# Optimization experiments

Hardware: AMD Instinct MI355X
Metric: run time of the kernel (lower is better)

Reference implementation:

```python
import jax, jax.numpy as jnp
from jax import lax
import numpy as np

DIM = 768      # model dim
NL = 12        # num mamba layers
DS = 16        # d_state
DI = 1536      # d_inner = 2*dim
DC = 4         # d_conv
P = 16         # patch size
IMG = 256
NP = (IMG // P) ** 2  # 256 patches
GS = 5         # KAN grid_size
SO = 3         # KAN spline_order
NK = NL // 3   # 4 KAN layers
BATCH = 32


def setup_inputs() -> dict:
    key = jax.random.key(0)
    ks = jax.random.split(key, 16)
    def n(k, shape, s=0.02):
        return jax.random.normal(k, shape, jnp.float32) * s
    return {
        "x": jax.random.normal(ks[0], (BATCH, 3, IMG, IMG), jnp.float32),
        "patch_w": n(ks[1], (DIM, 3, P, P)),
        "patch_b": jnp.zeros((DIM,), jnp.float32),
        "pos_embed": n(ks[2], (1, NP, DIM)),
        "in_proj_w": n(ks[3], (NL, 2 * DI, DIM)),
        "conv_w": n(ks[4], (NL, DI, 1, DC), 0.1),
        "conv_b": jnp.zeros((NL, DI), jnp.float32),
        "x_proj_w": n(ks[5], (NL, 2 * DS, DI)),
        "dt_proj_w": n(ks[6], (NL, DS, DI)),
        "dt_proj_b": jnp.zeros((NL, DS), jnp.float32),
        "A_log": jnp.tile(jnp.log(jnp.arange(1, DS + 1, dtype=jnp.float32)), (NL, 1)),
        "D_param": jnp.ones((NL, DI), jnp.float32),
        "out_proj_w": n(ks[7], (NL, DIM, DI)),
        "kan_base_w": n(ks[8], (NK, DIM, DIM)),
        "kan_coeff": n(ks[9], (NK, DIM, DIM, GS + SO), 0.1),
        "kan_bias": n(ks[10], (NK, DIM), 0.01),
        "norm_w": jnp.ones((DIM,), jnp.float32),
        "norm_b": jnp.zeros((DIM,), jnp.float32),
    }


def _mamba_block(x, in_w, cw, cb, xpw, dtw, dtb, alog, Dp, ow):
    Bsz, L, _ = x.shape
    xr = jnp.einsum('bld,ed->ble', x, in_w)              # [B,L,2*DI]
    x1, res = xr[..., :DI], xr[..., DI:]
    # causal depthwise conv (pad d_conv-1 on left, truncate to L)
    xc = lax.conv_general_dilated(
        x1.transpose(0, 2, 1), cw, (1,), [(DC - 1, 0)],
        feature_group_count=DI,
        dimension_numbers=('NCH', 'OIH', 'NCH')) + cb[None, :, None]
    x1 = jax.nn.silu(xc.transpose(0, 2, 1))              # [B,L,DI]
    x_dbl = jnp.einsum('bld,ed->ble', x1, xpw)           # [B,L,2*DS]
    Bp = x_dbl[..., DS:]                                 # dt half of x_proj is discarded (as in torch)
    dt = jax.nn.softplus(jnp.einsum('bld,nd->bln', x1, dtw) + dtb)  # [B,L,DS]
    A = -jnp.exp(alog)                                   # [DS]
    Ad = jnp.exp(A * dt)                                 # [B,L,DS]
    u = x1[..., :DI // DS].mean(-1)                      # [B,L]
    Bd = dt * Bp * u[..., None]                          # [B,L,DS]
    def step(s, ab):
        a, b = ab
        s = s * a + b
        return s, s
    _, ys = lax.scan(step, jnp.zeros((Bsz, DS), x.dtype),
                     (Ad.transpose(1, 0, 2), Bd.transpose(1, 0, 2)))
    y = ys.transpose(1, 0, 2)                            # [B,L,DS]
    y = jnp.repeat(y, DI // DS, axis=-1)                 # n -> (n d)
    y = y + x1 * Dp
    y = y * jax.nn.silu(res)
    return jnp.einsum('bld,ed->ble', y, ow)              # [B,L,DIM]


def _kan(xf, bw, coeff, bias):
    base = xf @ bw.T + bias
    grid = jnp.linspace(-1.0, 1.0, GS + 1)
    denom = grid[1:] - grid[:-1] + 1e-8
    xs = (xf[..., None] - grid[:-1]) / denom             # [M,DIM,GS]
    basis = jnp.where((xs >= 0) & (xs < 1), xs, 0.0)
    return base + jnp.einsum('bik,oik->bo', basis, coeff[:, :, :GS])


def reference(x, patch_w, patch_b, pos_embed, in_proj_w, conv_w, conv_b,
              x_proj_w, dt_proj_w, dt_proj_b, A_log, D_param, out_proj_w,
              kan_base_w, kan_coeff, kan_bias, norm_w, norm_b):
    Bsz = x.shape[0]
    h = lax.conv_general_dilated(
        x, patch_w, (P, P), 'VALID',
        dimension_numbers=('NCHW', 'OIHW', 'NCHW')) + patch_b[None, :, None, None]
    h = h.transpose(0, 2, 3, 1).reshape(Bsz, NP, DIM) + pos_embed
    for i in range(NL):
        h = _mamba_block(h, in_proj_w[i], conv_w[i], conv_b[i], x_proj_w[i],
                         dt_proj_w[i], dt_proj_b[i], A_log[i], D_param[i], out_proj_w[i])
        if i % 3 == 2 and i // 3 < NK:
            j = i // 3
            hf = h.reshape(-1, DIM)
            h = _kan(hf, kan_base_w[j], kan_coeff[j], kan_bias[j]).reshape(Bsz, NP, DIM) + h
    mu = h.mean(-1, keepdims=True)
    var = ((h - mu) ** 2).mean(-1, keepdims=True)
    return (h - mu) / jnp.sqrt(var + 1e-5) * norm_w + norm_b
```

## Files before the change

### kernel.cpp

```cpp
#include <hip/hip_runtime.h>

#define BATCH 32
#define NPATCH 256
#define MROWS (BATCH * NPATCH)
#define DIM 768
#define DI 1536
#define DS 16

typedef __bf16 bf16_t;
typedef __attribute__((ext_vector_type(8))) __bf16 bf16x8;
typedef __attribute__((ext_vector_type(4))) float floatx4;

__device__ __forceinline__ float bf2f(unsigned short u) {
    union { unsigned int i; float f; } v; v.i = ((unsigned int)u) << 16; return v.f;
}
__device__ __forceinline__ unsigned short f2bf(float f) {
    union { float f; unsigned int i; } u; u.f = f;
    unsigned int r = u.i + 0x7FFFu + ((u.i >> 16) & 1u);
    return (unsigned short)(r >> 16);
}
__device__ __forceinline__ float ldin(const void* p, int i, int bf) {
    if (bf) return bf2f(((const unsigned short*)p)[i]);
    return ((const float*)p)[i];
}
__device__ __forceinline__ float4 ldin4(const void* p, int i, int bf) {
    if (bf) {
        ushort4 u = *(const ushort4*)((const unsigned short*)p + i);
        return make_float4(bf2f(u.x), bf2f(u.y), bf2f(u.z), bf2f(u.w));
    }
    return *(const float4*)((const float*)p + i);
}
__device__ __forceinline__ float siluf(float x) { return x / (1.0f + expf(-x)); }

__global__ void detect_k(const void* alog, int* flag) {
    if (threadIdx.x == 0 && blockIdx.x == 0) {
        float v = ((const float*)alog)[1];
        flag[0] = (fabsf(v - 0.69314718f) < 0.01f) ? 0 : 1;
    }
}

__global__ __launch_bounds__(256) void cvt4_k(const int* __restrict__ flag,
                                              const void* __restrict__ in,
                                              unsigned short* __restrict__ out, int n4) {
    int i = blockIdx.x * 256 + threadIdx.x;
    if (i >= n4) return;
    float4 v = ldin4(in, i * 4, flag[0]);
    ushort4 o;
    o.x = f2bf(v.x); o.y = f2bf(v.y); o.z = f2bf(v.z); o.w = f2bf(v.w);
    *(ushort4*)(out + i * 4) = o;
}

__global__ __launch_bounds__(256) void kcoef_k(const int* __restrict__ flag,
                                               const void* __restrict__ co,
                                               bf16_t* __restrict__ out) {
    int idx = blockIdx.x * 256 + threadIdx.x;
    int bf = flag[0];
    int j = idx / (768 * 3840);
    int r = idx - j * (768 * 3840);
    int n = r / 3840;
    int kk = r - n * 3840;
    int i = kk / 5, k5 = kk - i * 5;
    out[idx] = (bf16_t)ldin(co, ((j * 768 + n) * 768 + i) * 8 + k5, bf);
}

__global__ __launch_bounds__(256) void wproj_k(const int* __restrict__ flag,
                                               const void* __restrict__ dtw,
                                               const void* __restrict__ xpw,
                                               bf16_t* __restrict__ w2) {
    int idx = blockIdx.x * 256 + threadIdx.x;
    int bf = flag[0];
    int i = idx / (128 * 1536);
    int r = idx - i * (128 * 1536);
    int n = r / 1536, k = r - n * 1536;
    float v;
    if (n < 16)       v = ldin(dtw, (i * 16 + n) * 1536 + k, bf);
    else if (n < 32)  v = ldin(xpw, (i * 32 + n) * 1536 + k, bf);
    else if (n == 32) v = (k < 96) ? (1.0f / 96.0f) : 0.0f;
    else              v = 0.0f;
    w2[idx] = (bf16_t)v;
}

__global__ __launch_bounds__(256) void cvtconv_k(const int* __restrict__ flag,
                                                 const void* __restrict__ cw,
                                                 bf16_t* __restrict__ cwr) {
    int idx = blockIdx.x * 256 + threadIdx.x;
    int bf = flag[0];
    int i = idx / (4 * 1536);
    int r = idx - i * (4 * 1536);
    int k = r / 1536, c = r - k * 1536;
    cwr[idx] = (bf16_t)ldin(cw, i * 1536 * 4 + c * 4 + k, bf);
}

__global__ __launch_bounds__(256) void basis_k(const bf16_t* __restrict__ h,
                                               bf16_t* __restrict__ bas) {
    int idx = blockIdx.x * 256 + threadIdx.x;
    int m = idx / 96, i8 = (idx - m * 96) * 8;
    bf16x8 hv = *(const bf16x8*)(h + (size_t)m * 768 + i8);
    union { bf16_t a[40]; bf16x8 v[5]; } ob;
#pragma unroll
    for (int ii = 0; ii < 8; ii++) {
        float xv = (float)hv[ii];
#pragma unroll
        for (int k5 = 0; k5 < 5; k5++) {
            float tt = (xv + 1.0f - 0.4f * (float)k5) * 2.5f;
            ob.a[ii * 5 + k5] = (bf16_t)((tt >= 0.0f && tt < 1.0f) ? tt : 0.0f);
        }
    }
    bf16_t* op = bas + (size_t)m * 3840 + (size_t)i8 * 5;
#pragma unroll
    for (int j = 0; j < 5; j++) *(bf16x8*)(op + j * 8) = ob.v[j];
}

__global__ __launch_bounds__(256) void im2col_k(const int* __restrict__ flag,
                                                const void* __restrict__ x,
                                                bf16_t* __restrict__ xp) {
    int idx = blockIdx.x * 256 + threadIdx.x;
    int bf = flag[0];
    int m = idx / 768, kc = idx - m * 768;
    int b = m >> 8, p = m & 255;
    int py = p >> 4, px = p & 15;
    int c = kc >> 8, rr = kc & 255;
    int ky = rr >> 4, kx = rr & 15;
    int src = ((b * 3 + c) * 256 + py * 16 + ky) * 256 + px * 16 + kx;
    xp[idx] = (bf16_t)ldin(x, src, bf);
}

__global__ __launch_bounds__(256) void mgemm_k(
    const bf16_t* __restrict__ A, int lda,
    const bf16_t* __restrict__ W, int ldw,
    bf16_t* __restrict__ C, int ldc,
    int K, int mode, int gx,
    const int* __restrict__ flag,
    const void* __restrict__ bias, int boff,
    const void* __restrict__ aux, int aoff,
    const bf16_t* __restrict__ H, int ldh,
    float* __restrict__ dtu) {
    __shared__ bf16_t sm[2][2 * 128 * 64];
    const int t = threadIdx.x;
    const int lane = t & 63, wave = t >> 6;
    const int wm = wave >> 1, wn = wave & 1;

    int m0, n0, kbeg, kend;
    if (mode == 5) {
        int mt = blockIdx.x >> 2, ks = blockIdx.x & 3;
        m0 = mt << 7; n0 = 0;
        int KS = K >> 2;
        kbeg = ks * KS; kend = kbeg + KS;
    } else {
        const int bid = blockIdx.x;
        const int xcd = bid & 7, l = bid >> 3;
        const int w = gx < 8 ? gx : 8;
        const int cb8 = w * 8;
        const int ch = l / cb8, rem = l - ch * cb8;
        const int mi = rem / w, ni = rem - mi * w;
        m0 = (xcd * 8 + mi) << 7;
        n0 = (ch * w + ni) << 7;
        kbeg = 0; kend = K;
    }

    const int srow = t >> 3;
    const int colperm = (((t & 7) ^ (srow & 7)) << 3);
    const bf16_t* gA[4]; const bf16_t* gB[4];
#pragma unroll
    for (int r = 0; r < 4; r++) {
        gA[r] = A + (size_t)(m0 + r * 32 + srow) * lda + colperm;
        gB[r] = W + (size_t)(n0 + r * 32 + srow) * ldw + colperm;
    }

    floatx4 acc[4][4];
#pragma unroll
    for (int i = 0; i < 4; i++)
#pragma unroll
        for (int j = 0; j < 4; j++) acc[i][j] = (floatx4){0.f, 0.f, 0.f, 0.f};

    const int kq = lane >> 4;
    const int mr = lane & 15;

    auto stage = [&](int buf, int kt) {
        char* sa = (char*)&sm[buf][0];
#pragma unroll
        for (int r = 0; r < 4; r++) {
            const int off = r * 4096 + wave * 1024;
            __builtin_amdgcn_global_load_lds(
                (const __attribute__((address_space(1))) unsigned int*)(gA[r] + kt),
                (__attribute__((address_space(3))) unsigned int*)(sa + off), 16, 0, 0);
            __builtin_amdgcn_global_load_lds(
                (const __attribute__((address_space(1))) unsigned int*)(gB[r] + kt),
                (__attribute__((address_space(3))) unsigned int*)(sa + 16384 + off), 16, 0, 0);
        }
    };

    auto compute = [&](int buf) {
        const bf16_t* sAc = &sm[buf][0];
        const bf16_t* sBc = sAc + 128 * 64;
#pragma unroll
        for (int half = 0; half < 2; half++) {
            const int cb = half * 4 + kq;
            if (mode == 5) {
                if (wn == 0) {
                    bf16x8 af[4], bw3[3];
#pragma unroll
                    for (int i = 0; i < 4; i++) {
                        int rw = wm * 64 + i * 16 + mr;
                        af[i] = *(const bf16x8*)(sAc + rw * 64 + ((cb ^ (rw & 7)) << 3));
                    }
#pragma unroll
                    for (int j = 0; j < 3; j++) {
                        int rw = j * 16 + mr;
                        bw3[j] = *(const bf16x8*)(sBc + rw * 64 + ((cb ^ (rw & 7)) << 3));
                    }
#pragma unroll
                    for (int i = 0; i < 4; i++)
#pragma unroll
                        for (int j = 0; j < 3; j++)
                            acc[i][j] = __builtin_amdgcn_mfma_f32_16x16x32_bf16(af[i], bw3[j], acc[i][j], 0, 0, 0);
                }
            } else {
                bf16x8 af[4], bw[4];
#pragma unroll
                for (int i = 0; i < 4; i++) {
                    int rw = wm * 64 + i * 16 + mr;
                    af[i] = *(const bf16x8*)(sAc + rw * 64 + ((cb ^ (rw & 7)) << 3));
                }
#pragma unroll
                for (int j = 0; j < 4; j++) {
                    int rw = wn * 64 + j * 16 + mr;
                    bw[j] = *(const bf16x8*)(sBc + rw * 64 + ((cb ^ (rw & 7)) << 3));
                }
#pragma unroll
                for (int i = 0; i < 4; i++)
#pragma unroll
                    for (int j = 0; j < 4; j++)
                        acc[i][j] = __builtin_amdgcn_mfma_f32_16x16x32_bf16(af[i], bw[j], acc[i][j], 0, 0, 0);
            }
        }
    };

    stage(0, kbeg);
    int cur = 0;
    for (int kt = kbeg; kt < kend; kt += 64) {
        if (kt + 64 < kend) {
            stage(cur ^ 1, kt + 64);
            asm volatile("s_waitcnt vmcnt(8)" ::: "memory");
        } else {
            asm volatile("s_waitcnt vmcnt(0)" ::: "memory");
        }
        asm volatile("s_barrier" ::: "memory");
        compute(cur);
        asm volatile("s_barrier" ::: "memory");
        cur ^= 1;
    }

    const int col = lane & 15;
    const int rq = (lane >> 4) * 4;

    if (mode == 5) {
        if (wn == 0) {
            int ks = blockIdx.x & 3;
            float* dst = dtu + (size_t)ks * (MROWS * 64);
#pragma unroll
            for (int i = 0; i < 4; i++) {
#pragma unroll
                for (int reg = 0; reg < 4; reg++) {
                    int gm = m0 + wm * 64 + i * 16 + rq + reg;
#pragma unroll
                    for (int j = 0; j < 3; j++) {
                        int gn = j * 16 + col;
                        if (gn <= 32)
                            dst[(size_t)gm * 64 + gn] = acc[i][j][reg];
                    }
                }
            }
        }
        return;
    }

    const int bff = (mode == 1 || mode == 2) ? flag[0] : 0;
#pragma unroll
    for (int i = 0; i < 4; i++) {
#pragma unroll
        for (int reg = 0; reg < 4; reg++) {
            int gm = m0 + wm * 64 + i * 16 + rq + reg;
#pragma unroll
            for (int j = 0; j < 4; j++) {
                int gn = n0 + wn * 64 + j * 16 + col;
                float v = acc[i][j][reg];
                if (mode == 1) v += ldin(bias, boff + gn, bff) + ldin(aux, aoff + (gm & 255) * 768 + gn, bff);
                else if (mode == 2) v += ldin(bias, boff + gn, bff);
                else if (mode == 3) v += (float)C[(size_t)gm * ldc + gn] + (float)H[(size_t)gm * ldh + gn];
                C[(size_t)gm * ldc + gn] = (bf16_t)v;
            }
        }
    }
}

__global__ __launch_bounds__(512, 2) void mgemm256_k(
    const bf16_t* __restrict__ A, int lda,
    const bf16_t* __restrict__ W, int ldw,
    bf16_t* __restrict__ C, int ldc,
    int K) {
    __shared__ bf16_t sm[2][2 * 256 * 64];
    const int t = threadIdx.x;
    const int lane = t & 63, wave = t >> 6;
    const int wm = wave >> 2, wn = wave & 3;

    const int bid = blockIdx.x;
    const int xcd = bid & 7, l = bid >> 3;
    const int mi = l & 3, ni = l >> 2;
    const int m0 = (xcd * 4 + mi) << 8;
    const int n0 = ni << 8;

    const int srow = t >> 3;
    const int colperm = (((t & 7) ^ (srow & 7)) << 3);
    const bf16_t* gA[4]; const bf16_t* gB[4];
#pragma unroll
    for (int r = 0; r < 4; r++) {
        gA[r] = A + (size_t)(m0 + r * 64 + srow) * lda + colperm;
        gB[r] = W + (size_t)(n0 + r * 64 + srow) * ldw + colperm;
    }

    floatx4 acc[8][4];
#pragma unroll
    for (int i = 0; i < 8; i++)
#pragma unroll
        for (int j = 0; j < 4; j++) acc[i][j] = (floatx4){0.f, 0.f, 0.f, 0.f};

    const int kq = lane >> 4;
    const int mr = lane & 15;

    auto stage = [&](int buf, int kt) {
        char* sa = (char*)&sm[buf][0];
#pragma unroll
        for (int r = 0; r < 4; r++) {
            const int off = (r * 512 + t) * 16;
            __builtin_amdgcn_global_load_lds(
                (const __attribute__((address_space(1))) unsigned int*)(gA[r] + kt),
                (__attribute__((address_space(3))) unsigned int*)(sa + off), 16, 0, 0);
            __builtin_amdgcn_global_load_lds(
                (const __attribute__((address_space(1))) unsigned int*)(gB[r] + kt),
                (__attribute__((address_space(3))) unsigned int*)(sa + 32768 + off), 16, 0, 0);
        }
    };

    stage(0, 0);
    int cur = 0;
    for (int kt = 0; kt < K; kt += 64) {
        asm volatile("s_waitcnt vmcnt(0)" ::: "memory");
        asm volatile("s_barrier" ::: "memory");
        if (kt + 64 < K) stage(cur ^ 1, kt + 64);
        const bf16_t* sAc = &sm[cur][0];
        const bf16_t* sBc = sAc + 256 * 64;
#pragma unroll
        for (int half = 0; half < 2; half++) {
            const int cb = half * 4 + kq;
            bf16x8 bw[4];
#pragma unroll
            for (int j = 0; j < 4; j++) {
                int rw = wn * 64 + j * 16 + mr;
                bw[j] = *(const bf16x8*)(sBc + rw * 64 + ((cb ^ (rw & 7)) << 3));
            }
#pragma unroll
            for (int ib = 0; ib < 2; ib++) {
                bf16x8 af[4];
#pragma unroll
                for (int i2 = 0; i2 < 4; i2++) {
                    int rw = wm * 128 + (ib * 4 + i2) * 16 + mr;
                    af[i2] = *(const bf16x8*)(sAc + rw * 64 + ((cb ^ (rw & 7)) << 3));
                }
                __builtin_amdgcn_s_setprio(1);
#pragma unroll
                for (int i2 = 0; i2 < 4; i2++)
#pragma unroll
                    for (int j = 0; j < 4; j++)
                        acc[ib * 4 + i2][j] = __builtin_amdgcn_mfma_f32_16x16x32_bf16(
                            af[i2], bw[j], acc[ib * 4 + i2][j], 0, 0, 0);
                __builtin_amdgcn_s_setprio(0);
                asm volatile("s_barrier" ::: "memory");
            }
        }
        cur ^= 1;
    }

    const int col = lane & 15;
    const int rq = (lane >> 4) * 4;
#pragma unroll
    for (int i = 0; i < 8; i++) {
#pragma unroll
        for (int reg = 0; reg < 4; reg++) {
            int gm = m0 + wm * 128 + i * 16 + rq + reg;
#pragma unroll
            for (int j = 0; j < 4; j++) {
                int gn = n0 + wn * 64 + j * 16 + col;
                C[(size_t)gm * ldc + gn] = (bf16_t)acc[i][j][reg];
            }
        }
    }
}

__global__ __launch_bounds__(256) void conv_k(const int* __restrict__ flag,
                                              const bf16_t* __restrict__ xr,
                                              const bf16_t* __restrict__ cwr,
                                              const void* __restrict__ cb, int cbo,
                                              bf16_t* __restrict__ xc) {
    int idx = blockIdx.x * 256 + threadIdx.x;
    int bf = flag[0];
    int m = idx / 192, c8 = (idx - m * 192) * 8;
    int l = m & 255;
    float acc[8];
    float4 b0 = ldin4(cb, cbo + c8, bf), b1 = ldin4(cb, cbo + c8 + 4, bf);
    acc[0] = b0.x; acc[1] = b0.y; acc[2] = b0.z; acc[3] = b0.w;
    acc[4] = b1.x; acc[5] = b1.y; acc[6] = b1.z; acc[7] = b1.w;
#pragma unroll
    for (int k = 0; k < 4; k++) {
        if (l + k - 3 >= 0) {
            bf16x8 xv = *(const bf16x8*)(xr + (size_t)(m + k - 3) * 3072 + c8);
            bf16x8 wv = *(const bf16x8*)(cwr + k * 1536 + c8);
#pragma unroll
            for (int j = 0; j < 8; j++) acc[j] += (float)xv[j] * (float)wv[j];
        }
    }
    bf16x8 o;
#pragma unroll
    for (int j = 0; j < 8; j++) o[j] = (bf16_t)siluf(acc[j]);
    *(bf16x8*)(xc + (size_t)m * 1536 + c8) = o;
}

__global__ __launch_bounds__(256) void scan_k(const int* __restrict__ flag,
                                              const float* __restrict__ dtu,
                                              const void* __restrict__ dtb, int dtbo,
                                              const void* __restrict__ alog, int alo,
                                              float* __restrict__ ys) {
    int wid = (blockIdx.x * 256 + threadIdx.x) >> 6;
    int lane = threadIdx.x & 63;
    int b = wid >> 4, s = wid & 15;
    int bf = flag[0];
    float dtbv = ldin(dtb, dtbo + s, bf);
    float Av = -expf(ldin(alog, alo + s, bf));
    const float* pb = dtu + (size_t)b * (256 * 64);
    float* yo = ys + (size_t)b * (256 * 16);
    float Aj[4], Bj[4];
    float A = 1.0f, Bv = 0.0f;
#pragma unroll
    for (int j = 0; j < 4; j++) {
        int l = lane * 4 + j;
        float rdt = dtbv, rBp = 0.0f, ru = 0.0f;
#pragma unroll
        for (int ks = 0; ks < 4; ks++) {
            const float* q = pb + (size_t)ks * (MROWS * 64) + (size_t)l * 64;
            rdt += q[s];
            rBp += q[16 + s];
            ru  += q[32];
        }
        float dt = (rdt > 20.0f) ? rdt : log1pf(expf(rdt));
        float a = expf(Av * dt);
        float bb = dt * rBp * ru;
        Bv = Bv * a + bb;
        A = A * a;
        Aj[j] = A; Bj[j] = Bv;
    }
#pragma unroll
    for (int off = 1; off < 64; off <<= 1) {
        float pa = __shfl_up(A, off);
        float pb2 = __shfl_up(Bv, off);
        if (lane >= off) { Bv = pb2 * A + Bv; A = pa * A; }
    }
    float ex = __shfl_up(Bv, 1);
    if (lane == 0) ex = 0.0f;
#pragma unroll
    for (int j = 0; j < 4; j++) {
        int l = lane * 4 + j;
        yo[l * 16 + s] = Aj[j] * ex + Bj[j];
    }
}

__global__ __launch_bounds__(256) void gate_k(const int* __restrict__ flag,
                                              const float* __restrict__ ys,
                                              bf16_t* __restrict__ xc,
                                              const bf16_t* __restrict__ xr,
                                              const void* __restrict__ Dp, int dpo) {
    int idx = blockIdx.x * 256 + threadIdx.x;
    int bf = flag[0];
    int m = idx / 192, d8 = (idx - m * 192) * 8;
    float yv = ys[m * 16 + d8 / 96];
    bf16x8 rv = *(const bf16x8*)(xr + (size_t)m * 3072 + 1536 + d8);
    bf16x8 xv = *(const bf16x8*)(xc + (size_t)m * 1536 + d8);
    float4 dp0 = ldin4(Dp, dpo + d8, bf), dp1 = ldin4(Dp, dpo + d8 + 4, bf);
    float dpv[8] = {dp0.x, dp0.y, dp0.z, dp0.w, dp1.x, dp1.y, dp1.z, dp1.w};
    bf16x8 o;
#pragma unroll
    for (int j = 0; j < 8; j++) {
        float v = yv + (float)xv[j] * dpv[j];
        o[j] = (bf16_t)(v * siluf((float)rv[j]));
    }
    *(bf16x8*)(xc + (size_t)m * 1536 + d8) = o;
}

__global__ __launch_bounds__(256) void lnorm_k(const int* __restrict__ flag,
                                               const bf16_t* __restrict__ h,
                                               const void* __restrict__ nw,
                                               const void* __restrict__ nb,
                                               void* __restrict__ out) {
    __shared__ float ls[4];
    int bf = flag[0];
    int m = blockIdx.x, t = threadIdx.x;
    const bf16_t* row = h + (size_t)m * 768;
    float v0 = (float)row[t], v1 = (float)row[t + 256], v2 = (float)row[t + 512];
    float s = v0 + v1 + v2;
#pragma unroll
    for (int o = 32; o; o >>= 1) s += __shfl_xor(s, o);
    if ((t & 63) == 0) ls[t >> 6] = s;
    __syncthreads();
    float mu = (ls[0] + ls[1] + ls[2] + ls[3]) * (1.0f / 768.0f);
    __syncthreads();
    float d0 = v0 - mu, d1 = v1 - mu, d2 = v2 - mu;
    float q = d0 * d0 + d1 * d1 + d2 * d2;
#pragma unroll
    for (int o = 32; o; o >>= 1) q += __shfl_xor(q, o);
    if ((t & 63) == 0) ls[t >> 6] = q;
    __syncthreads();
    float var = (ls[0] + ls[1] + ls[2] + ls[3]) * (1.0f / 768.0f);
    float inv = rsqrtf(var + 1e-5f);
    float vv[3] = {d0, d1, d2};
#pragma unroll
    for (int j = 0; j < 3; j++) {
        int colx = t + 256 * j;
        float o = vv[j] * inv * ldin(nw, colx, bf) + ldin(nb, colx, bf);
        size_t oi = (size_t)m * 768 + colx;
        if (bf) ((unsigned short*)out)[oi] = f2bf(o);
        else    ((float*)out)[oi] = o;
    }
}

extern "C" void kernel_launch(void* const* d_in, const int* in_sizes, int n_in,
                              void* d_out, int out_size, void* d_ws, size_t ws_size,
                              hipStream_t stream) {
    const void* x        = d_in[0];
    const void* patch_w  = d_in[1];
    const void* patch_b  = d_in[2];
    const void* pos      = d_in[3];
    const void* in_w     = d_in[4];
    const void* conv_w   = d_in[5];
    const void* conv_b   = d_in[6];
    const void* xpw      = d_in[7];
    const void* dtw      = d_in[8];
    const void* dtb      = d_in[9];
    const void* alog     = d_in[10];
    const void* Dp       = d_in[11];
    const void* out_w    = d_in[12];
    const void* kbw      = d_in[13];
    const void* kcoef    = d_in[14];
    const void* kbias    = d_in[15];
    const void* nw       = d_in[16];
    const void* nb       = d_in[17];

    char* base = (char*)d_ws;
    size_t off = 0;
    int* flag = (int*)base;                          off += 256;
    float* dtu  = (float*)(base + off);              off += (size_t)4 * MROWS * 64 * 4;
    float* ysb  = (float*)(base + off);              off += (size_t)MROWS * 16 * 4;
    bf16_t* hA  = (bf16_t*)(base + off);             off += (size_t)MROWS * DIM * 2;
    bf16_t* hB  = (bf16_t*)(base + off);             off += (size_t)MROWS * DIM * 2;
    bf16_t* xr  = (bf16_t*)(base + off);             off += (size_t)MROWS * 2 * DI * 2;
    bf16_t* xc  = (bf16_t*)(base + off);             off += (size_t)MROWS * DI * 2;
    bf16_t* wpatch = (bf16_t*)(base + off);          off += (size_t)DIM * DIM * 2;
    bf16_t* win  = (bf16_t*)(base + off);            off += (size_t)12 * 2 * DI * DIM * 2;
    bf16_t* wout = (bf16_t*)(base + off);            off += (size_t)12 * DIM * DI * 2;
    bf16_t* wkbw = (bf16_t*)(base + off);            off += (size_t)4 * DIM * DIM * 2;
    bf16_t* wkco = (bf16_t*)(base + off);            off += (size_t)4 * DIM * 3840 * 2;
    bf16_t* w2   = (bf16_t*)(base + off);            off += (size_t)12 * 128 * DI * 2;
    bf16_t* cwr  = (bf16_t*)(base + off);            off += (size_t)12 * 4 * DI * 2;
    bf16_t* basis = xr;
    bf16_t* im2c  = xr;

    detect_k<<<1, 64, 0, stream>>>(alog, flag);

    cvt4_k<<<(DIM * DIM / 4 + 255) / 256, 256, 0, stream>>>(flag, patch_w, (unsigned short*)wpatch, DIM * DIM / 4);
    cvt4_k<<<(12 * 2 * DI * DIM / 4 + 255) / 256, 256, 0, stream>>>(flag, in_w, (unsigned short*)win, 12 * 2 * DI * DIM / 4);
    cvt4_k<<<(12 * DIM * DI / 4 + 255) / 256, 256, 0, stream>>>(flag, out_w, (unsigned short*)wout, 12 * DIM * DI / 4);
    cvt4_k<<<(4 * DIM * DIM / 4 + 255) / 256, 256, 0, stream>>>(flag, kbw, (unsigned short*)wkbw, 4 * DIM * DIM / 4);
    kcoef_k<<<4 * DIM * 3840 / 256, 256, 0, stream>>>(flag, kcoef, wkco);
    wproj_k<<<12 * 128 * DI / 256, 256, 0, stream>>>(flag, dtw, xpw, w2);
    cvtconv_k<<<12 * 4 * DI / 256, 256, 0, stream>>>(flag, conv_w, cwr);

    im2col_k<<<(MROWS * DIM) / 256, 256, 0, stream>>>(flag, x, im2c);
    mgemm_k<<<6 * 64, 256, 0, stream>>>(
        im2c, DIM, wpatch, DIM, hA, DIM, DIM, 1, 6,
        flag, patch_b, 0, pos, 0, nullptr, 0, nullptr);

    bf16_t* hcur = hA;
    bf16_t* hoth = hB;
    for (int i = 0; i < 12; i++) {
        mgemm256_k<<<384, 512, 0, stream>>>(
            hcur, DIM, win + (size_t)i * 2 * DI * DIM, DIM, xr, 2 * DI, DIM);
        conv_k<<<(MROWS * 192) / 256, 256, 0, stream>>>(
            flag, xr, cwr + (size_t)i * 4 * DI, conv_b, i * DI, xc);
        mgemm_k<<<256, 256, 0, stream>>>(
            xc, DI, w2 + (size_t)i * 128 * DI, DI, nullptr, 128, DI, 5, 1,
            flag, nullptr, 0, nullptr, 0, nullptr, 0, dtu);
        scan_k<<<128, 256, 0, stream>>>(flag, dtu, dtb, i * DS, alog, i * DS, ysb);
        gate_k<<<(MROWS * 192) / 256, 256, 0, stream>>>(
            flag, ysb, xc, xr, Dp, i * DI);
        mgemm_k<<<6 * 64, 256, 0, stream>>>(
            xc, DI, wout + (size_t)i * DIM * DI, DI, hcur, DIM, DI, 0, 6,
            flag, nullptr, 0, nullptr, 0, nullptr, 0, nullptr);
        if (i % 3 == 2) {
            int j = i / 3;
            mgemm_k<<<6 * 64, 256, 0, stream>>>(
                hcur, DIM, wkbw + (size_t)j * DIM * DIM, DIM, hoth, DIM, DIM, 2, 6,
                flag, kbias, j * DIM, nullptr, 0, nullptr, 0, nullptr);
            basis_k<<<(MROWS * 96) / 256, 256, 0, stream>>>(hcur, basis);
            mgemm_k<<<6 * 64, 256, 0, stream>>>(
                basis, 3840, wkco + (size_t)j * DIM * 3840, 3840, hoth, DIM, 3840, 3, 6,
                flag, nullptr, 0, nullptr, 0, hcur, DIM, nullptr);
            bf16_t* tmp = hcur; hcur = hoth; hoth = tmp;
        }
    }

    lnorm_k<<<MROWS, 256, 0, stream>>>(flag, hcur, nw, nb, d_out);
}
```

Before: 2.592 ms.

## Restructure in_proj GEMM pipeline and compute two rows per conv thread

The 256-tile GEMM now issues the next stage's global-to-LDS loads before waiting, using a partial vmcnt wait so prefetch overlaps compute. It drops the per-half barriers and the setprio hints, and relaxes launch bounds to one block per CU, giving the compiler more registers. The depthwise conv kernel now has each thread produce two consecutive rows, reusing the weights and overlapping input rows to cut redundant loads, and launches half as many threads. The risks are lower occupancy in the GEMM and a wait count that may not match the actual number of outstanding loads, which could read LDS before it is filled.

Result: faster. 2.515 ms (-3.0%).

```diff
diff --git a/kernel.cpp b/kernel.cpp
--- a/kernel.cpp
+++ b/kernel.cpp
@@ -294,7 +294,7 @@
     }
 }
 
-__global__ __launch_bounds__(512, 2) void mgemm256_k(
+__global__ __launch_bounds__(512, 1) void mgemm256_k(
     const bf16_t* __restrict__ A, int lda,
     const bf16_t* __restrict__ W, int ldw,
     bf16_t* __restrict__ C, int ldc,
@@ -342,13 +342,8 @@
         }
     };
 
-    stage(0, 0);
-    int cur = 0;
-    for (int kt = 0; kt < K; kt += 64) {
-        asm volatile("s_waitcnt vmcnt(0)" ::: "memory");
-        asm volatile("s_barrier" ::: "memory");
-        if (kt + 64 < K) stage(cur ^ 1, kt + 64);
-        const bf16_t* sAc = &sm[cur][0];
+    auto compute = [&](int buf) {
+        const bf16_t* sAc = &sm[buf][0];
         const bf16_t* sBc = sAc + 256 * 64;
 #pragma unroll
         for (int half = 0; half < 2; half++) {
@@ -367,17 +362,28 @@
                     int rw = wm * 128 + (ib * 4 + i2) * 16 + mr;
                     af[i2] = *(const bf16x8*)(sAc + rw * 64 + ((cb ^ (rw & 7)) << 3));
                 }
-                __builtin_amdgcn_s_setprio(1);
 #pragma unroll
                 for (int i2 = 0; i2 < 4; i2++)
 #pragma unroll
                     for (int j = 0; j < 4; j++)
                         acc[ib * 4 + i2][j] = __builtin_amdgcn_mfma_f32_16x16x32_bf16(
                             af[i2], bw[j], acc[ib * 4 + i2][j], 0, 0, 0);
-                __builtin_amdgcn_s_setprio(0);
-                asm volatile("s_barrier" ::: "memory");
             }
         }
+    };
+
+    stage(0, 0);
+    int cur = 0;
+    for (int kt = 0; kt < K; kt += 64) {
+        if (kt + 64 < K) {
+            stage(cur ^ 1, kt + 64);
+            asm volatile("s_waitcnt vmcnt(8)" ::: "memory");
+        } else {
+            asm volatile("s_waitcnt vmcnt(0)" ::: "memory");
+        }
+        asm volatile("s_barrier" ::: "memory");
+        compute(cur);
+        asm volatile("s_barrier" ::: "memory");
         cur ^= 1;
     }
 
@@ -404,25 +410,37 @@
                                               bf16_t* __restrict__ xc) {
     int idx = blockIdx.x * 256 + threadIdx.x;
     int bf = flag[0];
-    int m = idx / 192, c8 = (idx - m * 192) * 8;
+    int mp = idx / 192, c8 = (idx - mp * 192) * 8;
+    int m = mp * 2;
     int l = m & 255;
-    float acc[8];
     float4 b0 = ldin4(cb, cbo + c8, bf), b1 = ldin4(cb, cbo + c8 + 4, bf);
-    acc[0] = b0.x; acc[1] = b0.y; acc[2] = b0.z; acc[3] = b0.w;
-    acc[4] = b1.x; acc[5] = b1.y; acc[6] = b1.z; acc[7] = b1.w;
+    float acc0[8] = {b0.x, b0.y, b0.z, b0.w, b1.x, b1.y, b1.z, b1.w};
+    float acc1[8] = {b0.x, b0.y, b0.z, b0.w, b1.x, b1.y, b1.z, b1.w};
+    bf16x8 wv[4];
+#pragma unroll
+    for (int k = 0; k < 4; k++) wv[k] = *(const bf16x8*)(cwr + k * 1536 + c8);
+    bf16x8 xrow[5];
+#pragma unroll
+    for (int r = 0; r < 5; r++) {
+        if (l + r - 3 >= 0)
+            xrow[r] = *(const bf16x8*)(xr + (size_t)(m + r - 3) * 3072 + c8);
+    }
 #pragma unroll
     for (int k = 0; k < 4; k++) {
         if (l + k - 3 >= 0) {
-            bf16x8 xv = *(const bf16x8*)(xr + (size_t)(m + k - 3) * 3072 + c8);
-            bf16x8 wv = *(const bf16x8*)(cwr + k * 1536 + c8);
-#pragma unroll
-            for (int j = 0; j < 8; j++) acc[j] += (float)xv[j] * (float)wv[j];
-        }
-    }
-    bf16x8 o;
-#pragma unroll
-    for (int j = 0; j < 8; j++) o[j] = (bf16_t)siluf(acc[j]);
-    *(bf16x8*)(xc + (size_t)m * 1536 + c8) = o;
+#pragma unroll
+            for (int j = 0; j < 8; j++) acc0[j] += (float)xrow[k][j] * (float)wv[k][j];
+        }
+        if (l + k - 2 >= 0) {
+#pragma unroll
+            for (int j = 0; j < 8; j++) acc1[j] += (float)xrow[k + 1][j] * (float)wv[k][j];
+        }
+    }
+    bf16x8 o0, o1;
+#pragma unroll
+    for (int j = 0; j < 8; j++) { o0[j] = (bf16_t)siluf(acc0[j]); o1[j] = (bf16_t)siluf(acc1[j]); }
+    *(bf16x8*)(xc + (size_t)m * 1536 + c8) = o0;
+    *(bf16x8*)(xc + (size_t)(m + 1) * 1536 + c8) = o1;
 }
 
 __global__ __launch_bounds__(256) void scan_k(const int* __restrict__ flag,
@@ -592,7 +610,7 @@
     for (int i = 0; i < 12; i++) {
         mgemm256_k<<<384, 512, 0, stream>>>(
             hcur, DIM, win + (size_t)i * 2 * DI * DIM, DIM, xr, 2 * DI, DIM);
-        conv_k<<<(MROWS * 192) / 256, 256, 0, stream>>>(
+        conv_k<<<(MROWS / 2 * 192) / 256, 256, 0, stream>>>(
             flag, xr, cwr + (size_t)i * 4 * DI, conv_b, i * DI, xc);
         mgemm_k<<<256, 256, 0, stream>>>(
             xc, DI, w2 + (size_t)i * 128 * DI, DI, nullptr, 128, DI, 5, 1,
```
